# Kernel tuning notes

Hardware: AMD Instinct MI355X
Metric: run time of the kernel (lower is better)

## Reference

```python
import jax, jax.numpy as jnp
import numpy as np

N_SEQ, N_RES, C_M = 512, 384, 256
C_OUTER, C_Z = 32, 128
LN_EPS = 1e-5
EPS = 1e-3


def setup_inputs() -> dict:
    key = jax.random.key(0)
    ks = jax.random.split(key, 8)
    act = jax.random.normal(ks[0], (N_SEQ, N_RES, C_M), dtype=jnp.float32)
    # binary MSA mask (float, as used multiplicatively in the module)
    mask = (jax.random.uniform(ks[1], (N_SEQ, N_RES)) < 0.9).astype(jnp.float32)
    s = 1.0 / np.sqrt(C_M)
    left_w = jax.random.normal(ks[2], (C_M, C_OUTER), dtype=jnp.float32) * s
    left_b = jnp.zeros((C_OUTER,), dtype=jnp.float32)
    right_w = jax.random.normal(ks[3], (C_M, C_OUTER), dtype=jnp.float32) * s
    right_b = jnp.zeros((C_OUTER,), dtype=jnp.float32)
    # zero_init=False -> VarianceScaling(scale=2.0, fan_in=C_OUTER*C_OUTER)
    ow_s = np.sqrt(2.0 / (C_OUTER * C_OUTER))
    output_w = jax.random.normal(ks[4], (C_OUTER, C_OUTER, C_Z), dtype=jnp.float32) * ow_s
    output_b = jnp.zeros((C_Z,), dtype=jnp.float32)
    ln_scale = jnp.ones((C_M,), dtype=jnp.float32)
    ln_offset = jnp.zeros((C_M,), dtype=jnp.float32)
    return {
        "act": act, "mask": mask,
        "ln_scale": ln_scale, "ln_offset": ln_offset,
        "left_w": left_w, "left_b": left_b,
        "right_w": right_w, "right_b": right_b,
        "output_w": output_w, "output_b": output_b,
    }


def reference(act, mask, ln_scale, ln_offset, left_w, left_b, right_w, right_b, output_w, output_b):
    # act: [N_seq, N_res, c_m], mask: [N_seq, N_res]
    m = mask[..., None]
    mu = jnp.mean(act, axis=-1, keepdims=True)
    var = jnp.var(act, axis=-1, keepdims=True)
    act_n = (act - mu) * jax.lax.rsqrt(var + LN_EPS) * ln_scale + ln_offset
    left = m * (jnp.einsum('abm,mc->abc', act_n, left_w) + left_b)    # [a, b, c]
    right = m * (jnp.einsum('adm,me->ade', act_n, right_w) + right_b)  # [a, d, e]
    # outer product mean over sequence dim a: [b, d, c, e]
    inter = jnp.einsum('abc,ade->bdce', left, right)
    out = jnp.einsum('bdce,cef->bdf', inter, output_w) + output_b      # [b, d, f]
    norm = jnp.einsum('ab,ad->bd', mask, mask)[..., None]              # [b, d, 1]
    return out / (EPS + norm)
```

## Files before the change

### kernel.cpp

```cpp
#include <hip/hip_runtime.h>

#define N_SEQ 512
#define N_RES 384
#define C_M   256

typedef __bf16 bf16;
typedef __bf16 bf16x4 __attribute__((ext_vector_type(4)));
typedef __bf16 bf16x8 __attribute__((ext_vector_type(8)));
typedef float  f32x4  __attribute__((ext_vector_type(4)));
typedef float  f32x16 __attribute__((ext_vector_type(16)));

static __device__ __forceinline__ bf16x8 ld8(const bf16* p) {
  bf16x4 lo = *(const bf16x4*)p;
  bf16x4 hi = *(const bf16x4*)(p + 4);
  bf16x8 r;
  r[0] = lo[0]; r[1] = lo[1]; r[2] = lo[2]; r[3] = lo[3];
  r[4] = hi[0]; r[5] = hi[1]; r[6] = hi[2]; r[7] = hi[3];
  return r;
}


__global__ void aux_kernel(const float* __restrict__ mask,
                           const float* __restrict__ lw, const float* __restrict__ rw,
                           const float* __restrict__ ow,
                           const float* __restrict__ ln_scale, const float* __restrict__ ln_offset,
                           const float* __restrict__ left_b, const float* __restrict__ right_b,
                           bf16* __restrict__ projW2, bf16* __restrict__ WtEp,
                           float* __restrict__ Svec, float* __restrict__ bias2,
                           float* __restrict__ recip) {
  int blk = blockIdx.x, t = threadIdx.x;
  if (blk < 576) {
    int bx = blk % 24, by = blk / 24;
    int b = bx * 16 + (t & 15), d = by * 16 + (t >> 4);
    float s = 0.f;
#pragma unroll 8
    for (int a = 0; a < N_SEQ; ++a)
      s += mask[a * N_RES + b] * mask[a * N_RES + d];
    recip[b * N_RES + d] = 1.0f / (1e-3f + s);
  } else if (blk < 1088) {
    int i2 = (blk - 576) * 256 + t;
    int f = i2 >> 10, k = i2 & 1023, e = k >> 5, c = k & 31;
    WtEp[i2] = (bf16)ow[(c * 32 + e) * 128 + f];
  } else if (blk < 1152) {
    int idx = (blk - 1088) * 256 + t;
    int o = idx >> 8, m = idx & 255;
    float w = (o < 32) ? lw[m * 32 + o] : rw[m * 32 + (o - 32)];
    projW2[idx] = (bf16)(ln_scale[m] * w);
  } else {
    if (t < 64) {
      int o = t;
      float s = 0.f, b2 = (o < 32) ? left_b[o] : right_b[o - 32];
      for (int m = 0; m < 256; ++m) {
        float w = (o < 32) ? lw[m * 32 + o] : rw[m * 32 + (o - 32)];
        s += (float)(bf16)(ln_scale[m] * w);
        b2 += ln_offset[m] * w;
      }
      Svec[o] = s; bias2[o] = b2;
    }
  }
}

__launch_bounds__(256)
__global__ void ln_project_kernel(const float* __restrict__ act, const float* __restrict__ mask,
                                  const bf16* __restrict__ projW2,
                                  const float* __restrict__ Svec, const float* __restrict__ bias2,
                                  bf16* __restrict__ leftT, bf16* __restrict__ rightT) {
  __shared__ __align__(16) bf16 At[128 * 264];
  __shared__ float2 muRow[128];
  bf16* outbuf = At;

  const int t = threadIdx.x;
  const int b = blockIdx.y;
  const int a0 = blockIdx.x * 128;
  const int wv = t >> 6, lane = t & 63;
  const int q = lane >> 4, l15 = lane & 15;

#pragma unroll 4
  for (int it = 0; it < 32; ++it) {
    const int row = it * 4 + wv;
    float4 v = *(const float4*)(act + ((size_t)(a0 + row) * N_RES + b) * C_M + lane * 4);
    bf16x4 r;
    r[0] = (bf16)v.x; r[1] = (bf16)v.y; r[2] = (bf16)v.z; r[3] = (bf16)v.w;
    *(bf16x4*)&At[row * 264 + lane * 4] = r;
  }
  __syncthreads();

  {
    int row = t >> 1, half = t & 1;
    const bf16* base = At + row * 264 + half * 128;
    float s1 = 0.f, s2 = 0.f;
#pragma unroll
    for (int i = 0; i < 16; ++i) {
      int ch = ((i + row) & 15) * 8;
      bf16x8 v = *(const bf16x8*)(base + ch);
#pragma unroll
      for (int u = 0; u < 8; ++u) { float x = (float)v[u]; s1 += x; s2 += x * x; }
    }
    s1 += __shfl_xor(s1, 1);
    s2 += __shfl_xor(s2, 1);
    if (half == 0) {
      float mean = s1 * (1.f / 256.f);
      float var  = s2 * (1.f / 256.f) - mean * mean;
      muRow[row] = make_float2(mean, rsqrtf(var + 1e-5f));
    }
  }

  f32x4 acc[2][4] = {};
#pragma unroll
  for (int s = 0; s < 8; ++s) {
    bf16x8 af[2], bfr[4];
#pragma unroll
    for (int i = 0; i < 2; ++i)
      af[i] = *(bf16x8*)&At[(wv * 32 + i * 16 + l15) * 264 + s * 32 + q * 8];
#pragma unroll
    for (int j = 0; j < 4; ++j)
      bfr[j] = *(const bf16x8*)&projW2[(j * 16 + l15) * 256 + s * 32 + q * 8];
#pragma unroll
    for (int i = 0; i < 2; ++i)
#pragma unroll
      for (int j = 0; j < 4; ++j)
        acc[i][j] = __builtin_amdgcn_mfma_f32_16x16x32_bf16(af[i], bfr[j], acc[i][j], 0, 0, 0);
  }
  __syncthreads();

  float Sv[4], Bv[4];
#pragma unroll
  for (int j = 0; j < 4; ++j) { Sv[j] = Svec[j * 16 + l15]; Bv[j] = bias2[j * 16 + l15]; }
#pragma unroll
  for (int i = 0; i < 2; ++i) {
#pragma unroll
    for (int r = 0; r < 4; ++r) {
      int a_local = wv * 32 + i * 16 + q * 4 + r;
      float2 ms = muRow[a_local];
      float mv = mask[(size_t)(a0 + a_local) * N_RES + b];
#pragma unroll
      for (int j = 0; j < 4; ++j) {
        float val = (ms.y * (acc[i][j][r] - ms.x * Sv[j]) + Bv[j]) * mv;
        outbuf[(j * 16 + l15) * 136 + a_local] = (bf16)val;
      }
    }
  }
  __syncthreads();

  {
    int o = t >> 2, part = t & 3;
    bf16* dst = (o < 32) ? (leftT + (size_t)(b * 32 + o) * 512)
                         : (rightT + (size_t)(b * 32 + (o - 32)) * 512);
#pragma unroll
    for (int v = 0; v < 4; ++v) {
      int asub = part * 32 + v * 8;
      bf16x8 val = *(bf16x8*)&outbuf[o * 136 + asub];
      *(bf16x8*)(dst + a0 + asub) = val;
    }
  }
}

__launch_bounds__(512, 2)
__global__ void outer_kernel(const bf16* __restrict__ leftT, const bf16* __restrict__ rightT,
                             const bf16* __restrict__ WtEp, const float* __restrict__ output_b,
                             const float* __restrict__ recip, float* __restrict__ out) {
  __shared__ __align__(16) union {
    bf16 A[256 * 68];
    bf16 Aep[64 * 1156];
    float P[4 * 64 * 2 * 64];
  } sm;

  const int t = threadIdx.x;
  const int sq = blockIdx.x >> 4, wi = blockIdx.x & 15;
  const int m0 = ((sq % 12) * 4 + (wi & 3)) * 256;
  const int n0 = ((sq / 12) * 4 + (wi >> 2)) * 256;

  const int wv = t >> 6, lane = t & 63;
  const int q = lane >> 4, l15 = lane & 15;
  const int l31 = lane & 31, h = lane >> 5;
  const int wm = (wv & 1) * 128, wn = (wv >> 1) * 64;

  const int srow = wv * 32 + (lane >> 3);
  const int skc  = lane & 7;
  const int sphys = skc ^ (lane >> 3);

  f32x16 acc[4][2] = {};
  uint4 areg[4];
#pragma unroll
  for (int w = 0; w < 4; ++w)
    areg[w] = *(const uint4*)(leftT + (size_t)(m0 + srow + w * 8) * 512 + skc * 8);

  for (int ks = 0; ks < 8; ++ks) {
    __syncthreads();
#pragma unroll
    for (int w = 0; w < 4; ++w) {
      int off = (srow + w * 8) * 68 + sphys * 8;
      *(uint2*)&sm.A[off]     = make_uint2(areg[w].x, areg[w].y);
      *(uint2*)&sm.A[off + 4] = make_uint2(areg[w].z, areg[w].w);
    }
    __syncthreads();
    if (ks < 7) {
#pragma unroll
      for (int w = 0; w < 4; ++w)
        areg[w] = *(const uint4*)(leftT + (size_t)(m0 + srow + w * 8) * 512 + (ks + 1) * 64 + skc * 8);
    }
    const bf16* Bbase = rightT + (size_t)(n0 + wn) * 512 + ks * 64 + h * 8;
    bf16x8 bc0 = *(const bf16x8*)(Bbase + (size_t)l31 * 512);
    bf16x8 bc1 = *(const bf16x8*)(Bbase + (size_t)(32 + l31) * 512);
#pragma unroll
    for (int s = 0; s < 4; ++s) {
      bf16x8 bn0, bn1;
      if (s < 3) {
        bn0 = *(const bf16x8*)(Bbase + (size_t)l31 * 512 + (s + 1) * 16);
        bn1 = *(const bf16x8*)(Bbase + (size_t)(32 + l31) * 512 + (s + 1) * 16);
      }
      bf16x8 af[4];
      int kc = s * 2 + h;
#pragma unroll
      for (int i = 0; i < 4; ++i)
        af[i] = ld8(&sm.A[(wm + i * 32 + l31) * 68 + ((kc ^ (l31 & 7)) * 8)]);
#pragma unroll
      for (int i = 0; i < 4; ++i) {
        acc[i][0] = __builtin_amdgcn_mfma_f32_32x32x16_bf16(af[i], bc0, acc[i][0], 0, 0, 0);
        acc[i][1] = __builtin_amdgcn_mfma_f32_32x32x16_bf16(af[i], bc1, acc[i][1], 0, 0, 0);
      }
      bc0 = bn0; bc1 = bn1;
    }
  }
  __syncthreads();

#pragma unroll
  for (int i = 0; i < 4; ++i) {
#pragma unroll
    for (int j = 0; j < 2; ++j) {
      int pair = ((wv & 1) * 4 + i) * 8 + (wv >> 1) * 2 + j;
      int base = pair * 1156 + l31 * 36;
#pragma unroll
      for (int g = 0; g < 4; ++g) {
        bf16x4 v;
        v[0] = (bf16)acc[i][j][4 * g + 0];
        v[1] = (bf16)acc[i][j][4 * g + 1];
        v[2] = (bf16)acc[i][j][4 * g + 2];
        v[3] = (bf16)acc[i][j][4 * g + 3];
        *(bf16x4*)&sm.Aep[base + 8 * g + 4 * h] = v;
      }
    }
  }
  __syncthreads();

  const int kq = wv & 3, fh = wv >> 2;
  f32x4 eacc[4][4] = {};
#pragma unroll
  for (int si = 0; si < 8; ++si) {
    int e = kq * 8 + si;
    bf16x8 wf[4];
#pragma unroll
    for (int j = 0; j < 4; ++j)
      wf[j] = *(const bf16x8*)&WtEp[(size_t)(fh * 64 + j * 16 + l15) * 1024 + e * 32 + q * 8];
    bf16x8 af[4];
#pragma unroll
    for (int mt = 0; mt < 4; ++mt)
      af[mt] = ld8(&sm.Aep[(mt * 16 + l15) * 1156 + e * 36 + q * 8]);
#pragma unroll
    for (int mt = 0; mt < 4; ++mt)
#pragma unroll
      for (int j = 0; j < 4; ++j)
        eacc[mt][j] = __builtin_amdgcn_mfma_f32_16x16x32_bf16(af[mt], wf[j], eacc[mt][j], 0, 0, 0);
  }
  __syncthreads();

#pragma unroll
  for (int mt = 0; mt < 4; ++mt)
#pragma unroll
    for (int j = 0; j < 4; ++j)
#pragma unroll
      for (int r = 0; r < 4; ++r) {
        int pair = mt * 16 + q * 4 + r;
        int fl = j * 16 + l15;
        sm.P[((kq * 64 + pair) * 2 + fh) * 64 + fl] = eacc[mt][j][r];
      }
  __syncthreads();

#pragma unroll
  for (int gg = 0; gg < 4; ++gg) {
    int g = t + 512 * gg;
    int pair = g >> 5, f4 = g & 31;
    int f = f4 * 4, fh2 = f >> 6, fl = f & 63;
    f32x4 s = {};
#pragma unroll
    for (int k2 = 0; k2 < 4; ++k2)
      s += *(f32x4*)&sm.P[((k2 * 64 + pair) * 2 + fh2) * 64 + fl];
    int b = (m0 >> 5) + (pair >> 3);
    int d = (n0 >> 5) + (pair & 7);
    float rc = recip[b * N_RES + d];
    float4 ob = *(const float4*)(output_b + f);
    f32x4 o;
    o[0] = (s[0] + ob.x) * rc; o[1] = (s[1] + ob.y) * rc;
    o[2] = (s[2] + ob.z) * rc; o[3] = (s[3] + ob.w) * rc;
    *(f32x4*)(out + ((size_t)b * N_RES + d) * 128 + f) = o;
  }
}

extern "C" void kernel_launch(void* const* d_in, const int* in_sizes, int n_in,
                              void* d_out, int out_size, void* d_ws, size_t ws_size,
                              hipStream_t stream) {
  const float* act       = (const float*)d_in[0];
  const float* mask      = (const float*)d_in[1];
  const float* ln_scale  = (const float*)d_in[2];
  const float* ln_offset = (const float*)d_in[3];
  const float* left_w    = (const float*)d_in[4];
  const float* left_b    = (const float*)d_in[5];
  const float* right_w   = (const float*)d_in[6];
  const float* right_b   = (const float*)d_in[7];
  const float* output_w  = (const float*)d_in[8];
  const float* output_b  = (const float*)d_in[9];
  float* out = (float*)d_out;

  char* ws = (char*)d_ws;
  bf16* leftT   = (bf16*)(ws);
  bf16* rightT  = (bf16*)(ws + 12582912);
  bf16* WtEp    = (bf16*)(ws + 25165824);
  bf16* projW2  = (bf16*)(ws + 25427968);
  float* Svec   = (float*)(ws + 25460736);
  float* bias2  = (float*)(ws + 25460992);
  float* recip  = (float*)(ws + 25461248);

  hipLaunchKernelGGL(aux_kernel, dim3(1153), dim3(256), 0, stream,
                     mask, left_w, right_w, output_w, ln_scale, ln_offset,
                     left_b, right_b, projW2, WtEp, Svec, bias2, recip);
  hipLaunchKernelGGL(ln_project_kernel, dim3(4, 384), dim3(256), 0, stream,
                     act, mask, projW2, Svec, bias2, leftT, rightT);
  hipLaunchKernelGGL(outer_kernel, dim3(2304), dim3(512), 0, stream,
                     leftT, rightT, WtEp, output_b, recip, out);
}
```

Baseline: 634.7 us.

## Stage A and B tiles via async global_load_lds with double-buffered pipeline

The outer-product GEMM loop now stages both the left and right operand tiles into LDS with direct global-to-LDS loads into a double-buffered, swizzled layout. Before, A went through registers into LDS and B was read straight from global memory. Loads for later k-steps are issued ahead and waited on with explicit vmcnt waits and barriers, and MFMA sections run at raised priority. This is meant to hide global latency and cut register staging, at the cost of more LDS use, many barriers per k-step, and fragile hand-tuned waitcnt ordering.

```diff
diff --git a/kernel.cpp b/kernel.cpp
--- a/kernel.cpp
+++ b/kernel.cpp
@@ -17,6 +17,10 @@
   r[0] = lo[0]; r[1] = lo[1]; r[2] = lo[2]; r[3] = lo[3];
   r[4] = hi[0]; r[5] = hi[1]; r[6] = hi[2]; r[7] = hi[3];
   return r;
+}
+
+template <int N> __device__ __forceinline__ void wait_vm() {
+  __builtin_amdgcn_s_waitcnt(N | (7 << 4) | (15 << 8));
 }
 
 
@@ -160,66 +164,80 @@
                              const bf16* __restrict__ WtEp, const float* __restrict__ output_b,
                              const float* __restrict__ recip, float* __restrict__ out) {
   __shared__ __align__(16) union {
-    bf16 A[256 * 68];
+    bf16 AB[8 * 8192];
     bf16 Aep[64 * 1156];
     float P[4 * 64 * 2 * 64];
   } sm;
 
-  const int t = threadIdx.x;
+  const int t_ = threadIdx.x;
   const int sq = blockIdx.x >> 4, wi = blockIdx.x & 15;
   const int m0 = ((sq % 12) * 4 + (wi & 3)) * 256;
   const int n0 = ((sq / 12) * 4 + (wi >> 2)) * 256;
 
-  const int wv = t >> 6, lane = t & 63;
+  const int wv = t_ >> 6, lane = t_ & 63;
   const int q = lane >> 4, l15 = lane & 15;
   const int l31 = lane & 31, h = lane >> 5;
   const int wm = (wv & 1) * 128, wn = (wv >> 1) * 64;
 
-  const int srow = wv * 32 + (lane >> 3);
-  const int skc  = lane & 7;
-  const int sphys = skc ^ (lane >> 3);
+  const int stR  = wv * 32 + (lane >> 2);
+  const int stKC = ((lane & 3) ^ ((lane >> 3) & 3)) * 8;
+  const int rsw  = (l31 >> 1) & 3;
+
+  const bf16* gA = leftT  + (size_t)m0 * 512;
+  const bf16* gB = rightT + (size_t)n0 * 512;
+
+#define BLK(d, mat, hf) ((((d) * 2 + (mat)) * 2 + (hf)) * 8192)
+#define STAGE(mat, T, hf) do {                                                              \
+    const bf16* _g = (mat) ? gB : gA;                                                       \
+    bf16* _l = sm.AB + BLK((T) & 1, mat, hf);                                               \
+    _Pragma("unroll")                                                                       \
+    for (int _j = 0; _j < 2; ++_j) {                                                        \
+      const bf16* _s = _g + (size_t)(stR + _j * 16) * 512 + (T) * 64 + (hf) * 32 + stKC;    \
+      __builtin_amdgcn_global_load_lds(                                                     \
+          (const __attribute__((address_space(1))) void*)_s,                                \
+          (__attribute__((address_space(3))) void*)(_l + (wv * 2 + _j) * 512), 16, 0, 0);   \
+    }                                                                                       \
+  } while (0)
 
   f32x16 acc[4][2] = {};
-  uint4 areg[4];
-#pragma unroll
-  for (int w = 0; w < 4; ++w)
-    areg[w] = *(const uint4*)(leftT + (size_t)(m0 + srow + w * 8) * 512 + skc * 8);
-
-  for (int ks = 0; ks < 8; ++ks) {
-    __syncthreads();
-#pragma unroll
-    for (int w = 0; w < 4; ++w) {
-      int off = (srow + w * 8) * 68 + sphys * 8;
-      *(uint2*)&sm.A[off]     = make_uint2(areg[w].x, areg[w].y);
-      *(uint2*)&sm.A[off + 4] = make_uint2(areg[w].z, areg[w].w);
-    }
-    __syncthreads();
-    if (ks < 7) {
-#pragma unroll
-      for (int w = 0; w < 4; ++w)
-        areg[w] = *(const uint4*)(leftT + (size_t)(m0 + srow + w * 8) * 512 + (ks + 1) * 64 + skc * 8);
-    }
-    const bf16* Bbase = rightT + (size_t)(n0 + wn) * 512 + ks * 64 + h * 8;
-    bf16x8 bc0 = *(const bf16x8*)(Bbase + (size_t)l31 * 512);
-    bf16x8 bc1 = *(const bf16x8*)(Bbase + (size_t)(32 + l31) * 512);
+
+  STAGE(0, 0, 0); STAGE(1, 0, 0);
+  STAGE(0, 0, 1); STAGE(1, 0, 1);
+  STAGE(0, 1, 0); STAGE(1, 1, 0);
+  wait_vm<8>();
+  __builtin_amdgcn_s_barrier();
+
+#pragma unroll
+  for (int t = 0; t < 8; ++t) {
 #pragma unroll
     for (int s = 0; s < 4; ++s) {
-      bf16x8 bn0, bn1;
-      if (s < 3) {
-        bn0 = *(const bf16x8*)(Bbase + (size_t)l31 * 512 + (s + 1) * 16);
-        bn1 = *(const bf16x8*)(Bbase + (size_t)(32 + l31) * 512 + (s + 1) * 16);
-      }
-      bf16x8 af[4];
-      int kc = s * 2 + h;
+      if (s == 0) { if (t < 7) STAGE(0, t + 1, 1); }
+      if (s == 1) { if (t < 7) STAGE(1, t + 1, 1); }
+      if (s == 2) { if (t < 6) STAGE(0, t + 2, 0); }
+      if (s == 3) { if (t < 6) STAGE(1, t + 2, 0); }
+
+      const bf16* Ab = sm.AB + BLK(t & 1, 0, s >> 1);
+      const bf16* Bb = sm.AB + BLK(t & 1, 1, s >> 1);
+      const int coff = (((s & 1) * 2 + h) ^ rsw) * 8;
+      bf16x8 af[4], b0, b1;
 #pragma unroll
       for (int i = 0; i < 4; ++i)
-        af[i] = ld8(&sm.A[(wm + i * 32 + l31) * 68 + ((kc ^ (l31 & 7)) * 8)]);
+        af[i] = *(const bf16x8*)&Ab[(wm + i * 32 + l31) * 32 + coff];
+      b0 = *(const bf16x8*)&Bb[(wn + l31) * 32 + coff];
+      b1 = *(const bf16x8*)&Bb[(wn + 32 + l31) * 32 + coff];
+
+      if (s == 1) { if (t < 7) wait_vm<8>(); else wait_vm<0>(); }
+      if (s == 3) { if (t < 6) wait_vm<8>(); else if (t == 6) wait_vm<4>(); }
+
+      __builtin_amdgcn_s_barrier();
+      __builtin_amdgcn_s_setprio(1);
 #pragma unroll
       for (int i = 0; i < 4; ++i) {
-        acc[i][0] = __builtin_amdgcn_mfma_f32_32x32x16_bf16(af[i], bc0, acc[i][0], 0, 0, 0);
-        acc[i][1] = __builtin_amdgcn_mfma_f32_32x32x16_bf16(af[i], bc1, acc[i][1], 0, 0, 0);
-      }
-      bc0 = bn0; bc1 = bn1;
+        acc[i][0] = __builtin_amdgcn_mfma_f32_32x32x16_bf16(af[i], b0, acc[i][0], 0, 0, 0);
+        acc[i][1] = __builtin_amdgcn_mfma_f32_32x32x16_bf16(af[i], b1, acc[i][1], 0, 0, 0);
+      }
+      __builtin_amdgcn_s_setprio(0);
+      __builtin_amdgcn_s_barrier();
     }
   }
   __syncthreads();
@@ -278,7 +296,7 @@
 
 #pragma unroll
   for (int gg = 0; gg < 4; ++gg) {
-    int g = t + 512 * gg;
+    int g = t_ + 512 * gg;
     int pair = g >> 5, f4 = g & 31;
     int f = f4 * 4, fh2 = f >> 6, fl = f & 63;
     f32x4 s = {};
```

After: 601.3 us. 5.3% less time.
